# Kernel tuning notes

Measured on AMD Instinct MI355X. Metric: run time of the kernel, lower is better.

## Reference

```python
import jax, jax.numpy as jnp
import numpy as np

N_ATOMS = 200_000   # total atoms across the batch of structures
D_IN = 256          # input feature dim
D_OUT = 256         # per-species expert output dim
N_SPECIES = 4       # number of atomic species (experts)
N_STRUCT = 2_000    # number of structures (segments for index_add)


def setup_inputs() -> dict:
    key = jax.random.key(0)
    k0, k1, k2, k3, k4 = jax.random.split(key, 5)
    x = jax.random.normal(k0, (N_ATOMS, D_IN), dtype=jnp.float32)
    # per-species expert weights (the 'models' ModuleDict -> Linear per specie)
    W = jax.random.normal(k1, (N_SPECIES, D_IN, D_OUT), dtype=jnp.float32) * (1.0 / np.float32(np.sqrt(D_IN)))
    b = jax.random.normal(k2, (N_SPECIES, D_OUT), dtype=jnp.float32) * 0.01
    central_species = jax.random.randint(k3, (N_ATOMS,), 0, N_SPECIES, dtype=jnp.int32)
    structural_indices = jnp.sort(jax.random.randint(k4, (N_ATOMS,), 0, N_STRUCT, dtype=jnp.int32))
    return {"x": x, "W": W, "b": b,
            "central_species": central_species,
            "structural_indices": structural_indices}


def reference(x, W, b, central_species, structural_indices):
    # CentralSplitter -> per-species expert (Linear) -> CentralUniter,
    # expressed as masked dense compute (same math per atom as gather/scatter):
    # each atom's row goes through exactly the expert of its species.
    n_species = W.shape[0]
    out = jnp.zeros((x.shape[0], W.shape[2]), dtype=x.dtype)
    for s in range(n_species):  # small fixed expert loop
        mask = (central_species == s)[:, None]
        out = out + jnp.where(mask, x @ W[s] + b[s], jnp.zeros((), x.dtype))
    # Accumulator: index_add over structural_indices == segment sum per structure
    return jax.ops.segment_sum(out, structural_indices, num_segments=N_STRUCT)
```

## Files before the change

kernel.cpp:

```cpp
#include <hip/hip_runtime.h>
#include <hip/hip_bf16.h>

#define N_ATOMS   200000
#define D_IN      256
#define D_OUT     256
#define N_SPECIES 4
#define N_STRUCT  2000
#define M_PAD     2048
#define KFLAT     1024
#define SEG_D     16

typedef __attribute__((ext_vector_type(8))) short bf16x8;
typedef __attribute__((ext_vector_type(4))) float f32x4;

typedef const __attribute__((address_space(1))) float gfloat;
typedef __attribute__((address_space(3))) float lfloat;

__device__ inline unsigned short f2bf(float f) {
    unsigned int u = __float_as_uint(f);
    unsigned int r = (u + 0x7fffu + ((u >> 16) & 1u)) >> 16;
    return (unsigned short)r;
}


__global__ void k_wt2(const float* __restrict__ W, unsigned short* __restrict__ Wt) {
    int gid = blockIdx.x * 256 + threadIdx.x;
    int o   = gid * 4;
    int kbg = o >> 14;
    int nn  = (o >> 6) & 255;
    int kp  = o & 63;
    int s   = kbg >> 2, kb = kbg & 3;
    int k0  = kb * 64 + kp;
    const float* wb = W + (size_t)s * 65536 + (size_t)k0 * 256 + nn;
    ushort4 u;
    u.x = f2bf(wb[0]);
    u.y = f2bf(wb[256]);
    u.z = f2bf(wb[512]);
    u.w = f2bf(wb[768]);
    *(ushort4*)(Wt + o) = u;
}

__device__ __forceinline__ int lb64(const int* __restrict__ sidx, int key, int lane) {
    int lo = 0, hi = N_ATOMS;
    while (hi - lo > 64) {
        int step = (hi - lo + 63) >> 6;
        int pos  = lo + lane * step;
        int v    = (pos < hi) ? sidx[pos] : 0x7fffffff;
        unsigned long long m = __ballot(v < key);
        int c = __popcll(m);
        int nlo = (c == 0)  ? lo : (lo + (c - 1) * step + 1);
        int nhi = (c == 64) ? hi : min(hi, lo + c * step);
        lo = nlo; hi = nhi;
    }
    int pos = lo + lane;
    int v   = (pos < hi) ? sidx[pos] : 0x7fffffff;
    unsigned long long m = __ballot(v < key);
    return lo + __popcll(m);
}

__global__ __launch_bounds__(256) void k_seg6(
        const float* __restrict__ x, const int* __restrict__ spec,
        const int* __restrict__ sidx, unsigned short* __restrict__ S,
        float* __restrict__ cnt) {

    __shared__ __align__(16) float ring[4][SEG_D][256];

    int t = threadIdx.x, w = t >> 6, lane = t & 63;
    int g = blockIdx.x * 4 + w;
    if (g >= N_STRUCT) return;

    int s0 = lb64(sidx, g,     lane);
    int s1 = lb64(sidx, g + 1, lane);
    int n  = s1 - s0;

    f32x4 a0 = (f32x4){0.f,0.f,0.f,0.f}, a1 = a0, a2 = a0, a3 = a0;
    float c0 = 0.f, c1 = 0.f, c2 = 0.f, c3 = 0.f;

    if (n > 0) {
        int nm1 = n - 1;
        const float* gp0 = x + (size_t)s0 * 256 + lane * 4;

        unsigned long long m0[4], m1[4];
        bool fits = (n <= 256);
        if (fits) {
#pragma unroll
            for (int c = 0; c < 4; ++c) {
                int sv = spec[s0 + min(c * 64 + lane, nm1)];
                m0[c] = __ballot((sv & 1) != 0);
                m1[c] = __ballot((sv & 2) != 0);
            }
        }

        asm volatile("s_waitcnt vmcnt(0)" ::: "memory");

#pragma unroll
        for (int j = 0; j < 15; ++j) {
            int rr = min(j, nm1);
            __builtin_amdgcn_global_load_lds(
                (gfloat*)(gp0 + (size_t)rr * 256),
                (lfloat*)&ring[w][j][0], 16, 0, 0);
        }

#define CONS4(vv, sp)                                                     \
        switch (sp) {                                                     \
            case 0: a0 += vv; c0 += 1.f; break;                           \
            case 1: a1 += vv; c1 += 1.f; break;                           \
            case 2: a2 += vv; c2 += 1.f; break;                           \
            default: a3 += vv; c3 += 1.f; break; }

        if (fits) {
#pragma unroll
            for (int c = 0; c < 4; ++c) {
                int cb = c * 64;
                if (cb < n) {
                    unsigned long long mm0 = m0[c], mm1 = m1[c];
                    int ce = min(n, cb + 64);
                    for (int j = cb; j < ce; ++j) {
                        asm volatile("s_waitcnt vmcnt(14)" ::: "memory");
                        f32x4 v = *(const f32x4*)&ring[w][j & (SEG_D - 1)][lane * 4];
                        int r  = j - cb;
                        int sp = (int)((mm0 >> r) & 1ull) | ((int)((mm1 >> r) & 1ull) << 1);
                        CONS4(v, sp);
                        int rr = min(j + 15, nm1);
                        __builtin_amdgcn_global_load_lds(
                            (gfloat*)(gp0 + (size_t)rr * 256),
                            (lfloat*)&ring[w][(j + 15) & (SEG_D - 1)][0], 16, 0, 0);
                    }
                }
            }
        } else {
            for (int cb = 0; cb < n; cb += 64) {
                int spv = spec[s0 + min(cb + lane, nm1)];
                asm volatile("s_waitcnt vmcnt(0)" ::: "memory");
                unsigned long long mm0 = __ballot((spv & 1) != 0);
                unsigned long long mm1 = __ballot((spv & 2) != 0);
                int ce = min(n, cb + 64);
                for (int j = cb; j < ce; ++j) {
                    f32x4 v = *(const f32x4*)&ring[w][j & (SEG_D - 1)][lane * 4];
                    int r  = j - cb;
                    int sp = (int)((mm0 >> r) & 1ull) | ((int)((mm1 >> r) & 1ull) << 1);
                    CONS4(v, sp);
                    int rr = min(j + 15, nm1);
                    __builtin_amdgcn_global_load_lds(
                        (gfloat*)(gp0 + (size_t)rr * 256),
                        (lfloat*)&ring[w][(j + 15) & (SEG_D - 1)][0], 16, 0, 0);
                    asm volatile("s_waitcnt vmcnt(14)" ::: "memory");
                }
            }
        }
#undef CONS4
    }

    unsigned short* Sg = S + (size_t)g * KFLAT + lane * 4;
    ushort4 u;
    u.x = f2bf(a0[0]); u.y = f2bf(a0[1]); u.z = f2bf(a0[2]); u.w = f2bf(a0[3]);
    *(ushort4*)(Sg + 0)   = u;
    u.x = f2bf(a1[0]); u.y = f2bf(a1[1]); u.z = f2bf(a1[2]); u.w = f2bf(a1[3]);
    *(ushort4*)(Sg + 256) = u;
    u.x = f2bf(a2[0]); u.y = f2bf(a2[1]); u.z = f2bf(a2[2]); u.w = f2bf(a2[3]);
    *(ushort4*)(Sg + 512) = u;
    u.x = f2bf(a3[0]); u.y = f2bf(a3[1]); u.z = f2bf(a3[2]); u.w = f2bf(a3[3]);
    *(ushort4*)(Sg + 768) = u;

    if (lane == 0) {
        float4 c4; c4.x = c0; c4.y = c1; c4.z = c2; c4.w = c3;
        *(float4*)(cnt + (size_t)g * 4) = c4;
    }
}

__global__ __launch_bounds__(256) void k_gemm4(
        const unsigned short* __restrict__ S, const float* __restrict__ cnt,
        const float* __restrict__ b, const unsigned short* __restrict__ Wt,
        float* __restrict__ out) {

    __shared__ __align__(16) f32x4 red[3 * 4 * 64];

    int t = threadIdx.x, w = t >> 6, lane = t & 63;
    int l15 = lane & 15, l4 = lane >> 4;
    int bid = blockIdx.x;
    int g0 = (bid >> 2) * 16;
    int c0 = (bid & 3) * 64;

    f32x4 acc[4];
#pragma unroll
    for (int n = 0; n < 4; ++n) acc[n] = (f32x4){0.f, 0.f, 0.f, 0.f};

    const unsigned short* arow = S + (size_t)(g0 + l15) * KFLAT + w * 256 + l4 * 8;
    const unsigned short* wsp  = Wt + (size_t)w * 4 * 16384 + l4 * 8;

#pragma unroll
    for (int kb = 0; kb < 4; ++kb) {
#pragma unroll
        for (int ks = 0; ks < 2; ++ks) {
            bf16x8 af = *(const bf16x8*)(arow + kb * 64 + ks * 32);
#pragma unroll
            for (int n = 0; n < 4; ++n) {
                bf16x8 bfr = *(const bf16x8*)(wsp + (size_t)kb * 16384
                                + (size_t)(c0 + n * 16 + l15) * 64 + ks * 32);
                acc[n] = __builtin_amdgcn_mfma_f32_16x16x32_bf16(af, bfr, acc[n], 0, 0, 0);
            }
        }
    }

    if (w > 0) {
#pragma unroll
        for (int n = 0; n < 4; ++n) red[(w - 1) * 256 + n * 64 + lane] = acc[n];
    }
    __syncthreads();
    if (w == 0) {
#pragma unroll
        for (int n = 0; n < 4; ++n)
            acc[n] += red[0 * 256 + n * 64 + lane]
                    + red[1 * 256 + n * 64 + lane]
                    + red[2 * 256 + n * 64 + lane];

        float bv[4][4];
#pragma unroll
        for (int n = 0; n < 4; ++n) {
            int col = c0 + n * 16 + l15;
#pragma unroll
            for (int s = 0; s < 4; ++s) bv[n][s] = b[s * 256 + col];
        }

#pragma unroll
        for (int r = 0; r < 4; ++r) {
            int grow = g0 + l4 * 4 + r;
            if (grow < N_STRUCT) {
                float4 c4 = *(const float4*)(cnt + (size_t)grow * 4);
#pragma unroll
                for (int n = 0; n < 4; ++n) {
                    int col = c0 + n * 16 + l15;
                    out[(size_t)grow * 256 + col] =
                        acc[n][r] + c4.x * bv[n][0] + c4.y * bv[n][1]
                                  + c4.z * bv[n][2] + c4.w * bv[n][3];
                }
            }
        }
    }
}

extern "C" void kernel_launch(void* const* d_in, const int* in_sizes, int n_in,
                              void* d_out, int out_size, void* d_ws, size_t ws_size,
                              hipStream_t stream) {
    const float* x    = (const float*)d_in[0];
    const float* W    = (const float*)d_in[1];
    const float* b    = (const float*)d_in[2];
    const int* spec   = (const int*)d_in[3];
    const int* sidx   = (const int*)d_in[4];
    float* out        = (float*)d_out;

    char* ws = (char*)d_ws;
    unsigned short* Wt = (unsigned short*)ws;
    unsigned short* S  = (unsigned short*)(ws + 524288);
    float* cnt  = (float*)(ws + 4718592);

    k_wt2  <<<512, 256, 0, stream>>>(W, Wt);
    k_seg6 <<<(N_STRUCT + 3) / 4, 256, 0, stream>>>(x, spec, sidx, S, cnt);
    k_gemm4<<<(M_PAD / 16) * (D_OUT / 64), 256, 0, stream>>>(S, cnt, b, Wt, out);
}
```

Baseline: 59.84 us.

## Fuse weight conversion into segment kernel and retile gemm to 32x32 blocks

```diff
diff --git a/kernel.cpp b/kernel.cpp
--- a/kernel.cpp
+++ b/kernel.cpp
@@ -9,6 +9,7 @@
 #define M_PAD     2048
 #define KFLAT     1024
 #define SEG_D     16
+#define WT_BLOCKS 512
 
 typedef __attribute__((ext_vector_type(8))) short bf16x8;
 typedef __attribute__((ext_vector_type(4))) float f32x4;
@@ -22,23 +23,6 @@
     return (unsigned short)r;
 }
 
-
-__global__ void k_wt2(const float* __restrict__ W, unsigned short* __restrict__ Wt) {
-    int gid = blockIdx.x * 256 + threadIdx.x;
-    int o   = gid * 4;
-    int kbg = o >> 14;
-    int nn  = (o >> 6) & 255;
-    int kp  = o & 63;
-    int s   = kbg >> 2, kb = kbg & 3;
-    int k0  = kb * 64 + kp;
-    const float* wb = W + (size_t)s * 65536 + (size_t)k0 * 256 + nn;
-    ushort4 u;
-    u.x = f2bf(wb[0]);
-    u.y = f2bf(wb[256]);
-    u.z = f2bf(wb[512]);
-    u.w = f2bf(wb[768]);
-    *(ushort4*)(Wt + o) = u;
-}
 
 __device__ __forceinline__ int lb64(const int* __restrict__ sidx, int key, int lane) {
     int lo = 0, hi = N_ATOMS;
@@ -58,15 +42,37 @@
     return lo + __popcll(m);
 }
 
-__global__ __launch_bounds__(256) void k_seg6(
-        const float* __restrict__ x, const int* __restrict__ spec,
-        const int* __restrict__ sidx, unsigned short* __restrict__ S,
+__global__ __launch_bounds__(256) void k_fused(
+        const float* __restrict__ x, const float* __restrict__ W,
+        const int* __restrict__ spec, const int* __restrict__ sidx,
+        unsigned short* __restrict__ Wt, unsigned short* __restrict__ S,
         float* __restrict__ cnt) {
 
     __shared__ __align__(16) float ring[4][SEG_D][256];
 
-    int t = threadIdx.x, w = t >> 6, lane = t & 63;
-    int g = blockIdx.x * 4 + w;
+    int t = threadIdx.x;
+    int bid = blockIdx.x;
+
+    if (bid < WT_BLOCKS) {
+        int gid = bid * 256 + t;
+        int o   = gid * 4;
+        int kbg = o >> 14;
+        int nn  = (o >> 6) & 255;
+        int kp  = o & 63;
+        int s   = kbg >> 2, kb = kbg & 3;
+        int k0  = kb * 64 + kp;
+        const float* wb = W + (size_t)s * 65536 + (size_t)k0 * 256 + nn;
+        ushort4 u;
+        u.x = f2bf(wb[0]);
+        u.y = f2bf(wb[256]);
+        u.z = f2bf(wb[512]);
+        u.w = f2bf(wb[768]);
+        *(ushort4*)(Wt + o) = u;
+        return;
+    }
+
+    int w = t >> 6, lane = t & 63;
+    int g = (bid - WT_BLOCKS) * 4 + w;
     if (g >= N_STRUCT) return;
 
     int s0 = lb64(sidx, g,     lane);
@@ -168,22 +174,24 @@
     }
 }
 
-__global__ __launch_bounds__(256) void k_gemm4(
+__global__ __launch_bounds__(256) void k_gemm5(
         const unsigned short* __restrict__ S, const float* __restrict__ cnt,
         const float* __restrict__ b, const unsigned short* __restrict__ Wt,
         float* __restrict__ out) {
 
-    __shared__ __align__(16) f32x4 red[3 * 4 * 64];
+    __shared__ __align__(16) f32x4 red[4][2][2][64];
 
     int t = threadIdx.x, w = t >> 6, lane = t & 63;
     int l15 = lane & 15, l4 = lane >> 4;
     int bid = blockIdx.x;
-    int g0 = (bid >> 2) * 16;
-    int c0 = (bid & 3) * 64;
-
-    f32x4 acc[4];
-#pragma unroll
-    for (int n = 0; n < 4; ++n) acc[n] = (f32x4){0.f, 0.f, 0.f, 0.f};
+    int g0 = (bid >> 3) * 32;
+    int c0 = (bid & 7) * 32;
+
+    f32x4 acc[2][2];
+#pragma unroll
+    for (int m = 0; m < 2; ++m)
+#pragma unroll
+        for (int n = 0; n < 2; ++n) acc[m][n] = (f32x4){0.f, 0.f, 0.f, 0.f};
 
     const unsigned short* arow = S + (size_t)(g0 + l15) * KFLAT + w * 256 + l4 * 8;
     const unsigned short* wsp  = Wt + (size_t)w * 4 * 16384 + l4 * 8;
@@ -192,48 +200,45 @@
     for (int kb = 0; kb < 4; ++kb) {
 #pragma unroll
         for (int ks = 0; ks < 2; ++ks) {
-            bf16x8 af = *(const bf16x8*)(arow + kb * 64 + ks * 32);
-#pragma unroll
-            for (int n = 0; n < 4; ++n) {
+            bf16x8 af[2];
+#pragma unroll
+            for (int m = 0; m < 2; ++m)
+                af[m] = *(const bf16x8*)(arow + (size_t)m * 16 * KFLAT + kb * 64 + ks * 32);
+#pragma unroll
+            for (int n = 0; n < 2; ++n) {
                 bf16x8 bfr = *(const bf16x8*)(wsp + (size_t)kb * 16384
                                 + (size_t)(c0 + n * 16 + l15) * 64 + ks * 32);
-                acc[n] = __builtin_amdgcn_mfma_f32_16x16x32_bf16(af, bfr, acc[n], 0, 0, 0);
-            }
-        }
-    }
-
-    if (w > 0) {
-#pragma unroll
-        for (int n = 0; n < 4; ++n) red[(w - 1) * 256 + n * 64 + lane] = acc[n];
-    }
+#pragma unroll
+                for (int m = 0; m < 2; ++m)
+                    acc[m][n] = __builtin_amdgcn_mfma_f32_16x16x32_bf16(af[m], bfr, acc[m][n], 0, 0, 0);
+            }
+        }
+    }
+
+#pragma unroll
+    for (int m = 0; m < 2; ++m)
+#pragma unroll
+        for (int n = 0; n < 2; ++n) red[w][m][n][lane] = acc[m][n];
     __syncthreads();
-    if (w == 0) {
-#pragma unroll
-        for (int n = 0; n < 4; ++n)
-            acc[n] += red[0 * 256 + n * 64 + lane]
-                    + red[1 * 256 + n * 64 + lane]
-                    + red[2 * 256 + n * 64 + lane];
-
-        float bv[4][4];
-#pragma unroll
-        for (int n = 0; n < 4; ++n) {
-            int col = c0 + n * 16 + l15;
-#pragma unroll
-            for (int s = 0; s < 4; ++s) bv[n][s] = b[s * 256 + col];
-        }
+
+    {
+        int mw = w >> 1, nw = w & 1;
+        f32x4 sum = red[0][mw][nw][lane] + red[1][mw][nw][lane]
+                  + red[2][mw][nw][lane] + red[3][mw][nw][lane];
+
+        int col = c0 + nw * 16 + l15;
+        float bv[4];
+#pragma unroll
+        for (int s = 0; s < 4; ++s) bv[s] = b[s * 256 + col];
 
 #pragma unroll
         for (int r = 0; r < 4; ++r) {
-            int grow = g0 + l4 * 4 + r;
+            int grow = g0 + mw * 16 + l4 * 4 + r;
             if (grow < N_STRUCT) {
                 float4 c4 = *(const float4*)(cnt + (size_t)grow * 4);
-#pragma unroll
-                for (int n = 0; n < 4; ++n) {
-                    int col = c0 + n * 16 + l15;
-                    out[(size_t)grow * 256 + col] =
-                        acc[n][r] + c4.x * bv[n][0] + c4.y * bv[n][1]
-                                  + c4.z * bv[n][2] + c4.w * bv[n][3];
-                }
+                out[(size_t)grow * 256 + col] =
+                    sum[r] + c4.x * bv[0] + c4.y * bv[1]
+                           + c4.z * bv[2] + c4.w * bv[3];
             }
         }
     }
@@ -254,7 +259,6 @@
     unsigned short* S  = (unsigned short*)(ws + 524288);
     float* cnt  = (float*)(ws + 4718592);
 
-    k_wt2  <<<512, 256, 0, stream>>>(W, Wt);
-    k_seg6 <<<(N_STRUCT + 3) / 4, 256, 0, stream>>>(x, spec, sidx, S, cnt);
-    k_gemm4<<<(M_PAD / 16) * (D_OUT / 64), 256, 0, stream>>>(S, cnt, b, Wt, out);
-}
+    k_fused<<<WT_BLOCKS + (N_STRUCT + 3) / 4, 256, 0, stream>>>(x, W, spec, sidx, Wt, S, cnt);
+    k_gemm5<<<(M_PAD / 32) * (D_OUT / 32), 256, 0, stream>>>(S, cnt, b, Wt, out);
+}
```

New measurement: 54.40 us. 9.1% less time.
